# Performance work log

Measured on AMD Instinct MI355X. Metric: run time of the kernel, lower is better.

The kernel has to match this reference:

```python
import jax, jax.numpy as jnp
import numpy as np

B, S, D, NH, NKV, HD = 1, 2048, 4096, 32, 8, 128
SCALE = HD ** -0.5


def setup_inputs() -> dict:
    key = jax.random.key(0)
    ks = jax.random.split(key, 5)
    sd = D ** -0.5
    x = jax.random.normal(ks[0], (B, S, D), jnp.float32)
    Wq = jax.random.normal(ks[1], (D, NH * HD), jnp.float32) * sd
    Wk = jax.random.normal(ks[2], (D, NKV * HD), jnp.float32) * sd
    Wv = jax.random.normal(ks[3], (D, NKV * HD), jnp.float32) * sd
    Wo = jax.random.normal(ks[4], (NH * HD, D), jnp.float32) * sd
    # real rotary tables (rotate-half convention), shape [S, HD]
    inv_freq = 1.0 / (10000.0 ** (np.arange(0, HD, 2, dtype=np.float64) / HD))
    ang = np.outer(np.arange(S, dtype=np.float64), inv_freq)  # [S, HD//2]
    emb = np.concatenate([ang, ang], axis=-1)  # [S, HD]
    cos = jnp.asarray(np.cos(emb), jnp.float32)
    sin = jnp.asarray(np.sin(emb), jnp.float32)
    return dict(x=x, Wq=Wq, Wk=Wk, Wv=Wv, Wo=Wo, cos=cos, sin=sin)


def _rope(t, cos, sin):
    # t: [B,S,H,HD]; cos/sin: [S,HD]
    c = cos[None, :, None, :]
    s = sin[None, :, None, :]
    t1, t2 = jnp.split(t, 2, axis=-1)
    rot = jnp.concatenate([-t2, t1], axis=-1)
    return t * c + rot * s


def _to_i8(t):
    # per-vector absmax quantization over last dim
    scale = 127.0 / jnp.clip(jnp.max(jnp.abs(t), axis=-1, keepdims=True), 1e-5, None)
    q = jnp.clip(jnp.round(t * scale), -128.0, 127.0).astype(jnp.int8)
    return q, scale


def reference(x, Wq, Wk, Wv, Wo, cos, sin):
    q = (x @ Wq).reshape(B, S, NH, HD)
    k = (x @ Wk).reshape(B, S, NKV, HD)
    v = (x @ Wv).reshape(B, S, NKV, HD)
    q = _rope(q, cos, sin)
    k = _rope(k, cos, sin)
    q_i8, q_s = _to_i8(q)          # [B,S,NH,HD], [B,S,NH,1]
    k_i8, k_s = _to_i8(k)          # [B,S,NKV,HD], [B,S,NKV,1]
    rep = NH // NKV                # GQA expansion
    k_i8 = jnp.repeat(k_i8, rep, axis=2)
    k_s = jnp.repeat(k_s, rep, axis=2)
    v = jnp.repeat(v, rep, axis=2)
    # int8 QK^T accumulated in int32 (exact), then per-vector dequant
    scores = jnp.einsum('bshd,bthd->bhst', q_i8, k_i8,
                        preferred_element_type=jnp.int32).astype(jnp.float32)
    q_st = jnp.transpose(q_s, (0, 2, 1, 3))            # [B,NH,S,1]
    k_st = jnp.transpose(k_s, (0, 2, 3, 1))            # [B,NH,1,S]
    scores = scores * (SCALE / (q_st * k_st))
    # causal mask (seq > 1, no cache so total == S)
    mask = jnp.triu(jnp.full((S, S), -jnp.inf, jnp.float32), k=1)
    scores = scores + mask
    attn = jax.nn.softmax(scores, axis=-1)             # [B,NH,S,S]
    out = jnp.einsum('bhst,bthd->bshd', attn, v).reshape(B, S, NH * HD)
    return out @ Wo
```

## Files before the change

### kernel.cpp

```cpp
#include <hip/hip_runtime.h>
#include <hip/hip_bf16.h>

#define S_LEN 2048
#define DMODEL 4096
#define NH 32
#define NKV 8
#define HD 128
#define NQKV 6144
#define VOFF (DMODEL + NKV * HD)
#define ATT_SCALE_L2E 0.1275175213528852f

typedef __bf16 bf16x8 __attribute__((ext_vector_type(8)));
typedef __bf16 bf16x4 __attribute__((ext_vector_type(4)));
typedef float f32x4 __attribute__((ext_vector_type(4)));

template <bool B> struct BoolC { static constexpr bool value = B; };

__device__ __forceinline__ unsigned short f2b(float f) {
  union { float f; unsigned u; } a; a.f = f;
  unsigned u = a.u;
  return (unsigned short)((u + 0x7FFFu + ((u >> 16) & 1u)) >> 16);
}
__device__ __forceinline__ float b2f(unsigned short u) {
  union { unsigned u; float f; } a; a.u = (unsigned)u << 16; return a.f;
}

__device__ __forceinline__ void gl16(const unsigned short* g, unsigned short* l) {
  __builtin_amdgcn_global_load_lds(
      (const __attribute__((address_space(1))) unsigned int*)g,
      (__attribute__((address_space(3))) unsigned int*)l, 16, 0, 0);
}

__global__ __launch_bounds__(256) void k_prep(const float* __restrict__ x,
                                              const float* __restrict__ Wq,
                                              const float* __restrict__ Wk,
                                              const float* __restrict__ Wv,
                                              const float* __restrict__ Wo,
                                              unsigned short* __restrict__ xb,
                                              unsigned short* __restrict__ wqkv_t,
                                              unsigned short* __restrict__ wo_t) {
  __shared__ float tile[64][65];
  const int id = blockIdx.x;
  if (id >= 10240) {
    int i = (id - 10240) * 256 + threadIdx.x;
    float4 v = ((const float4*)x)[i];
    ushort4 o;
    o.x = f2b(v.x); o.y = f2b(v.y); o.z = f2b(v.z); o.w = f2b(v.w);
    ((ushort4*)xb)[i] = o;
    return;
  }
  const float* W;
  unsigned short* Wt;
  int N, bx, by;
  if (id < 4096)      { W = Wq; Wt = wqkv_t;                         N = 4096; bx = id & 63;          by = id >> 6; }
  else if (id < 5120) { W = Wk; Wt = wqkv_t + (size_t)4096 * 4096;   N = 1024; bx = (id - 4096) & 63; by = (id - 4096) >> 6; }
  else if (id < 6144) { W = Wv; Wt = wqkv_t + (size_t)5120 * 4096;   N = 1024; bx = (id - 5120) & 63; by = (id - 5120) >> 6; }
  else                { W = Wo; Wt = wo_t;                           N = 4096; bx = (id - 6144) & 63; by = (id - 6144) >> 6; }
  const int k0 = bx * 64, n0 = by * 64;
  const int tx = threadIdx.x & 31, ty = threadIdx.x >> 5;
#pragma unroll
  for (int i = 0; i < 8; ++i) {
    int k = ty + i * 8;
    const float* src = W + (size_t)(k0 + k) * N + n0;
    tile[k][tx] = src[tx];
    tile[k][tx + 32] = src[tx + 32];
  }
  __syncthreads();
  int kq = threadIdx.x & 15, nb = threadIdx.x >> 4;
#pragma unroll
  for (int i = 0; i < 4; ++i) {
    int n = nb + i * 16;
    ushort4 o;
    o.x = f2b(tile[kq * 4 + 0][n]);
    o.y = f2b(tile[kq * 4 + 1][n]);
    o.z = f2b(tile[kq * 4 + 2][n]);
    o.w = f2b(tile[kq * 4 + 3][n]);
    *(ushort4*)&Wt[(size_t)(n0 + n) * 4096 + k0 + kq * 4] = o;
  }
}

__global__ __launch_bounds__(256) void k_post(const unsigned short* __restrict__ qkv,
                                              const float* __restrict__ cost,
                                              const float* __restrict__ sint,
                                              unsigned short* __restrict__ q_int,
                                              float* __restrict__ q_ds_t,
                                              unsigned short* __restrict__ k_int,
                                              float* __restrict__ k_ds_t,
                                              unsigned short* __restrict__ v_t) {
  __shared__ unsigned short tile[64][65];
  const int id = blockIdx.x;
  if (id < 20480) {
    int y = id >> 11, s = id & 2047;
    int wv = threadIdx.x >> 6, l = threadIdx.x & 63;
    int hh = y * 4 + wv;
    const unsigned short* row = qkv + (size_t)s * NQKV;
    int off = (hh < NH) ? hh * HD : DMODEL + (hh - NH) * HD;
    float t1 = b2f(row[off + l]), t2 = b2f(row[off + 64 + l]);
    float c1 = cost[s * HD + l],      sn1 = sint[s * HD + l];
    float c2 = cost[s * HD + 64 + l], sn2 = sint[s * HD + 64 + l];
    float o1 = t1 * c1 - t2 * sn1;
    float o2 = t2 * c2 + t1 * sn2;
    float amax = fmaxf(fabsf(o1), fabsf(o2));
#pragma unroll
    for (int m = 1; m < 64; m <<= 1) amax = fmaxf(amax, __shfl_xor(amax, m));
    amax = fmaxf(amax, 1e-5f);
    float scale = 127.0f / amax;
    float dscale = amax * (1.0f / 127.0f);
    float v1 = fminf(fmaxf(rintf(o1 * scale), -128.f), 127.f);
    float v2 = fminf(fmaxf(rintf(o2 * scale), -128.f), 127.f);
    if (hh < NH) {
      unsigned short* dst = q_int + ((size_t)s * NH + hh) * HD;
      dst[l] = f2b(v1); dst[l + 64] = f2b(v2);
      if (l == 0) q_ds_t[(size_t)hh * S_LEN + s] = dscale;
    } else {
      int kh = hh - NH;
      unsigned short* dst = k_int + ((size_t)s * NKV + kh) * HD;
      dst[l] = f2b(v1); dst[l + 64] = f2b(v2);
      if (l == 0) k_ds_t[(size_t)kh * S_LEN + s] = dscale;
    }
    return;
  }
  int vid = id - 20480;
  int s0 = (vid & 31) * 64, d0 = ((vid >> 5) & 1) * 64, kvh = vid >> 6;
  int tx = threadIdx.x & 63, ty = threadIdx.x >> 6;
#pragma unroll
  for (int i = 0; i < 16; ++i) {
    int s = ty + i * 4;
    tile[s][tx] = qkv[(size_t)(s0 + s) * NQKV + VOFF + kvh * HD + d0 + tx];
  }
  __syncthreads();
#pragma unroll
  for (int i = 0; i < 16; ++i) {
    int d = ty + i * 4;
    v_t[((size_t)kvh * HD + d0 + d) * S_LEN + s0 + tx] = tile[tx][d];
  }
}

__global__ __launch_bounds__(512, 4) void k_g128x3(const unsigned short* __restrict__ A,
                                                   const unsigned short* __restrict__ B,
                                                   unsigned short* __restrict__ C,
                                                   int M, int N, int K) {
  constexpr int FN = 3;
  extern __shared__ __align__(16) unsigned short smem[];
  char* Sc = (char*)smem;
  const int tid = threadIdx.x;
  const int wvid = tid >> 6, l = tid & 63;
  const int wm = wvid >> 2, wn = wvid & 3;
  const int l15 = l & 15, l4 = l >> 4;

  const int cpx = gridDim.x >> 3;
  const int swz = (blockIdx.x & 7) * cpx + (blockIdx.x >> 3);
  const int mtiles = M >> 7;
  const int m0 = (swz % mtiles) * 128;
  const int n0 = (swz / mtiles) * (FN * 64);

  const int NT = K >> 6;

  const int rsw = (l15 & 7) << 4;
  const int a_base = (wm * 64 + l15) * 128;
  const int b_base = (wn * FN * 16 + l15) * 128;
  const int c0 = (l4 * 16) ^ rsw;
  const int c1 = (64 + l4 * 16) ^ rsw;

  const int srow = l >> 3;
  const int st_k8 = (l & 7) ^ (srow & 7);

  auto stA = [&](int tt) {
    if (tt >= NT) return;
    const unsigned short* g = A + (size_t)(m0 + wvid * 8 + srow) * K + tt * 64 + st_k8 * 8;
    char* lb = Sc + (tt & 1) * 16384 + wvid * 1024;
#pragma unroll
    for (int j = 0; j < 2; ++j)
      gl16(g + (size_t)(j * 64) * K, (unsigned short*)(lb + j * 8192));
  };
  auto stB = [&](int tt) {
    if (tt >= NT) return;
    const unsigned short* g = B + (size_t)(n0 + wvid * 8 + srow) * K + tt * 64 + st_k8 * 8;
    char* lb = Sc + 32768 + (tt & 1) * (FN * 8192) + wvid * 1024;
#pragma unroll
    for (int j = 0; j < FN; ++j)
      gl16(g + (size_t)(j * 64) * K, (unsigned short*)(lb + j * 8192));
  };

  f32x4 acc[4][FN] = {};

  stA(0); stB(0); stA(1);
  if (NT > 1) asm volatile("s_waitcnt vmcnt(2)" ::: "memory");
  else        asm volatile("s_waitcnt vmcnt(0)" ::: "memory");
  __builtin_amdgcn_s_barrier();

  for (int t = 0; t < NT; ++t) {
    const char* Ab = Sc + (t & 1) * 16384;
    const char* Bb = Sc + 32768 + (t & 1) * (FN * 8192);
    stB(t + 1);
    bf16x8 a[4], b[FN];
#pragma unroll
    for (int fm = 0; fm < 4; ++fm) a[fm] = *(const bf16x8*)(Ab + a_base + fm * 2048 + c0);
#pragma unroll
    for (int fn = 0; fn < FN; ++fn) b[fn] = *(const bf16x8*)(Bb + b_base + fn * 2048 + c0);
    __builtin_amdgcn_s_setprio(1);
#pragma unroll
    for (int fm = 0; fm < 4; ++fm)
#pragma unroll
      for (int fn = 0; fn < FN; ++fn)
        acc[fm][fn] = __builtin_amdgcn_mfma_f32_16x16x32_bf16(a[fm], b[fn], acc[fm][fn], 0, 0, 0);
    __builtin_amdgcn_s_setprio(0);
#pragma unroll
    for (int fm = 0; fm < 4; ++fm) a[fm] = *(const bf16x8*)(Ab + a_base + fm * 2048 + c1);
#pragma unroll
    for (int fn = 0; fn < FN; ++fn) b[fn] = *(const bf16x8*)(Bb + b_base + fn * 2048 + c1);
    __builtin_amdgcn_s_setprio(1);
#pragma unroll
    for (int fm = 0; fm < 4; ++fm)
#pragma unroll
      for (int fn = 0; fn < FN; ++fn)
        acc[fm][fn] = __builtin_amdgcn_mfma_f32_16x16x32_bf16(a[fm], b[fn], acc[fm][fn], 0, 0, 0);
    __builtin_amdgcn_s_setprio(0);
    __builtin_amdgcn_s_barrier();
    stA(t + 2);
    if (t + 1 < NT) {
      if (t + 1 == NT - 1) asm volatile("s_waitcnt vmcnt(0)" ::: "memory");
      else                 asm volatile("s_waitcnt vmcnt(2)" ::: "memory");
      __builtin_amdgcn_s_barrier();
    }
  }

#pragma unroll
  for (int fm = 0; fm < 4; ++fm) {
    int row0 = m0 + wm * 64 + fm * 16 + l4 * 4;
#pragma unroll
    for (int fn = 0; fn < FN; ++fn) {
      int col = n0 + wn * FN * 16 + fn * 16 + l15;
#pragma unroll
      for (int r = 0; r < 4; ++r)
        C[(size_t)(row0 + r) * N + col] = f2b(acc[fm][fn][r]);
    }
  }
}

__global__ __launch_bounds__(512, 4) void k_gksplit(const unsigned short* __restrict__ A,
                                                    const unsigned short* __restrict__ B,
                                                    float* __restrict__ C,
                                                    int M, int N, int K) {
  extern __shared__ __align__(16) unsigned short smem[];
  char* Sc = (char*)smem;
  const int tid = threadIdx.x;
  const int wvid = tid >> 6, l = tid & 63;
  const int wm = wvid & 1, wn = (wvid >> 1) & 1, wk = wvid >> 2;
  const int l15 = l & 15, l4 = l >> 4;

  const int cpx = gridDim.x >> 3;
  const int swz = (blockIdx.x & 7) * cpx + (blockIdx.x >> 3);
  const int mtiles = M >> 7;
  const int m0 = (swz % mtiles) * 128;
  const int n0 = (swz / mtiles) * 128;

  const int NT = K >> 6;

  const int rsw = (l15 & 7) << 4;
  const int a_base = (wm * 64 + l15) * 128;
  const int b_base = (wn * 64 + l15) * 128;
  const int ck = (wk * 64 + l4 * 16) ^ rsw;

  const int srow = l >> 3;
  const int st_k8 = (l & 7) ^ (srow & 7);

  auto stA = [&](int tt) {
    if (tt >= NT) return;
    const unsigned short* g = A + (size_t)(m0 + wvid * 8 + srow) * K + tt * 64 + st_k8 * 8;
    char* lb = Sc + (tt & 1) * 16384 + wvid * 1024;
#pragma unroll
    for (int j = 0; j < 2; ++j)
      gl16(g + (size_t)(j * 64) * K, (unsigned short*)(lb + j * 8192));
  };
  auto stB = [&](int tt) {
    if (tt >= NT) return;
    const unsigned short* g = B + (size_t)(n0 + wvid * 8 + srow) * K + tt * 64 + st_k8 * 8;
    char* lb = Sc + 32768 + (tt & 1) * 16384 + wvid * 1024;
#pragma unroll
    for (int j = 0; j < 2; ++j)
      gl16(g + (size_t)(j * 64) * K, (unsigned short*)(lb + j * 8192));
  };

  f32x4 acc[4][4] = {};

  stA(0); stB(0); stA(1);
  if (NT > 1) asm volatile("s_waitcnt vmcnt(2)" ::: "memory");
  else        asm volatile("s_waitcnt vmcnt(0)" ::: "memory");
  __builtin_amdgcn_s_barrier();

  for (int t = 0; t < NT; ++t) {
    const char* Ab = Sc + (t & 1) * 16384;
    const char* Bb = Sc + 32768 + (t & 1) * 16384;
    stB(t + 1);
    bf16x8 a[4], b[4];
#pragma unroll
    for (int fm = 0; fm < 4; ++fm) a[fm] = *(const bf16x8*)(Ab + a_base + fm * 2048 + ck);
#pragma unroll
    for (int fn = 0; fn < 4; ++fn) b[fn] = *(const bf16x8*)(Bb + b_base + fn * 2048 + ck);
    __builtin_amdgcn_s_setprio(1);
#pragma unroll
    for (int fm = 0; fm < 4; ++fm)
#pragma unroll
      for (int fn = 0; fn < 4; ++fn)
        acc[fm][fn] = __builtin_amdgcn_mfma_f32_16x16x32_bf16(a[fm], b[fn], acc[fm][fn], 0, 0, 0);
    __builtin_amdgcn_s_setprio(0);
    __builtin_amdgcn_s_barrier();
    stA(t + 2);
    if (t + 1 < NT) {
      if (t + 1 == NT - 1) asm volatile("s_waitcnt vmcnt(0)" ::: "memory");
      else                 asm volatile("s_waitcnt vmcnt(2)" ::: "memory");
      __builtin_amdgcn_s_barrier();
    }
  }

  char* xch = Sc + (wm * 2 + wn) * 16384;
  if (wk == 1) {
#pragma unroll
    for (int fm = 0; fm < 4; ++fm)
#pragma unroll
      for (int fn = 0; fn < 4; ++fn)
        *(f32x4*)(xch + (fm * 4 + fn) * 1024 + l * 16) = acc[fm][fn];
  }
  __syncthreads();
  if (wk == 0) {
#pragma unroll
    for (int fm = 0; fm < 4; ++fm) {
      int row0 = m0 + wm * 64 + fm * 16 + l4 * 4;
#pragma unroll
      for (int fn = 0; fn < 4; ++fn) {
        f32x4 o = *(const f32x4*)(xch + (fm * 4 + fn) * 1024 + l * 16);
        int col = n0 + wn * 64 + fn * 16 + l15;
#pragma unroll
        for (int r = 0; r < 4; ++r)
          C[(size_t)(row0 + r) * N + col] = acc[fm][fn][r] + o[r];
      }
    }
  }
}

__global__ __launch_bounds__(512, 4) void k_attn(const unsigned short* __restrict__ q_int,
                                                 const float* __restrict__ q_ds_t,
                                                 const unsigned short* __restrict__ k_int,
                                                 const float* __restrict__ k_ds_t,
                                                 const unsigned short* __restrict__ v_t,
                                                 unsigned short* __restrict__ o_bf) {
  __shared__ __align__(16) unsigned short K_lds[2][8192];
  __shared__ __align__(16) unsigned short V_lds[2][8192];
  __shared__ __align__(16) unsigned short P_lds[8][1024];

  const int bid = blockIdx.x;
  const int kvh = bid & 7;
  const int qt = 63 - (bid >> 3);
  const int tid = threadIdx.x, wv = tid >> 6, l = tid & 63;
  const int l15 = l & 15, l4 = l >> 4;
  const int h = kvh * 4 + (wv & 3);
  const int rh = wv >> 2;

  auto stage = [&](int b, int kt) {
    const unsigned short* kB = k_int + (size_t)kt * 64 * (NKV * HD) + kvh * HD;
    const unsigned short* vB = v_t + (size_t)kvh * HD * S_LEN + (size_t)kt * 64;
#pragma unroll
    for (int j = 0; j < 2; ++j) {
      int wi = j * 8 + wv;
      int slot = wi * 64 + l;
      int key = slot >> 4;
      int colb = ((slot & 15) * 16) ^ ((key & 7) << 4);
      gl16(kB + key * (NKV * HD) + (colb >> 1), &K_lds[b][wi * 512]);
      int d = slot >> 3;
      int ckb = ((slot & 7) * 16) ^ ((d & 7) << 4);
      gl16(vB + (size_t)d * S_LEN + (ckb >> 1), &V_lds[b][wi * 512]);
    }
  };

  const int qrow_lo = qt * 32 + rh * 16;
  const int qg = qrow_lo + l15;
  const int crow = qrow_lo + l4 * 4;

  bf16x8 qf[4];
  {
    const unsigned short* qp = q_int + ((size_t)qg * NH + h) * HD + l4 * 8;
#pragma unroll
    for (int kd = 0; kd < 4; ++kd) qf[kd] = *(const bf16x8*)(qp + kd * 32);
  }
  const float qsS = ATT_SCALE_L2E * q_ds_t[(size_t)h * S_LEN + qg];

  float m_run = -3.0e38f, l_run = 0.f;
  f32x4 o_acc[8] = {};

  const int nkt = (qt >> 1) + 1;
  stage(0, 0);
  __syncthreads();

  const int psw = (l15 & 7) << 4;

  auto tileBody = [&](auto mc, int kt) {
    constexpr bool MASKED = decltype(mc)::value;
    const int cur = kt & 1;
    f32x4 ksd[4];
    {
      const f32x4* kdp = (const f32x4*)(k_ds_t + (size_t)kvh * S_LEN + kt * 64 + l4 * 4);
#pragma unroll
      for (int nt = 0; nt < 4; ++nt) ksd[nt] = kdp[nt * 4];
    }
    if (kt + 1 < nkt) stage(cur ^ 1, kt + 1);

    f32x4 sacc[4] = {};
#pragma unroll
    for (int nt = 0; nt < 4; ++nt) {
      int key = nt * 16 + l15;
#pragma unroll
      for (int kd = 0; kd < 4; ++kd) {
        int byte = key * 256 + kd * 64 + l4 * 16;
        byte ^= (key & 7) << 4;
        bf16x8 kf = *(const bf16x8*)((const char*)&K_lds[cur][0] + byte);
        sacc[nt] = __builtin_amdgcn_mfma_f32_16x16x32_bf16(kf, qf[kd], sacc[nt], 0, 0, 0);
      }
    }

    float p[4][4];
    float tmax = -3.0e38f;
#pragma unroll
    for (int nt = 0; nt < 4; ++nt) {
#pragma unroll
      for (int r = 0; r < 4; ++r) {
        float sc = sacc[nt][r] * (qsS * ksd[nt][r]);
        if constexpr (MASKED) {
          int keyg = kt * 64 + nt * 16 + l4 * 4 + r;
          sc = (keyg <= qg) ? sc : -3.0e38f;
        }
        p[nt][r] = sc;
        tmax = fmaxf(tmax, sc);
      }
    }
    tmax = fmaxf(tmax, __shfl_xor(tmax, 16));
    tmax = fmaxf(tmax, __shfl_xor(tmax, 32));

    float nm = fmaxf(m_run, tmax);
    bool need = tmax > m_run + 11.0f;
    if (__ballot(need)) {
      float corr = __builtin_amdgcn_exp2f(m_run - nm);
      m_run = nm;
      l_run *= corr;
      float cq[4];
#pragma unroll
      for (int r = 0; r < 4; ++r) cq[r] = __shfl(corr, (l & 48) | (l4 * 4 + r));
#pragma unroll
      for (int dt = 0; dt < 8; ++dt)
#pragma unroll
        for (int r = 0; r < 4; ++r) o_acc[dt][r] *= cq[r];
    }

    float psum = 0.f;
#pragma unroll
    for (int nt = 0; nt < 4; ++nt)
#pragma unroll
      for (int r = 0; r < 4; ++r) {
        float e = __builtin_amdgcn_exp2f(p[nt][r] - m_run);
        p[nt][r] = e;
        psum += e;
      }
    psum += __shfl_xor(psum, 16);
    psum += __shfl_xor(psum, 32);
    l_run += psum;

#pragma unroll
    for (int nt = 0; nt < 4; ++nt) {
      bf16x4 pk;
      pk[0] = (__bf16)p[nt][0]; pk[1] = (__bf16)p[nt][1];
      pk[2] = (__bf16)p[nt][2]; pk[3] = (__bf16)p[nt][3];
      int bw = l15 * 128 + ((nt * 32 + l4 * 8) ^ psw);
      *(bf16x4*)((char*)&P_lds[wv][0] + bw) = pk;
    }
    bf16x8 pa[2];
#pragma unroll
    for (int kc = 0; kc < 2; ++kc) {
      int br = l15 * 128 + ((kc * 64 + l4 * 16) ^ psw);
      pa[kc] = *(const bf16x8*)((const char*)&P_lds[wv][0] + br);
    }

#pragma unroll
    for (int dt = 0; dt < 8; ++dt) {
      int d = dt * 16 + l15;
      int swzv = (d & 7) << 4;
#pragma unroll
      for (int kc = 0; kc < 2; ++kc) {
        int byte = d * 128 + ((kc * 64 + l4 * 16) ^ swzv);
        bf16x8 vb = *(const bf16x8*)((const char*)&V_lds[cur][0] + byte);
        o_acc[dt] = __builtin_amdgcn_mfma_f32_16x16x32_bf16(pa[kc], vb, o_acc[dt], 0, 0, 0);
      }
    }
    __syncthreads();
  };

  for (int kt = 0; kt + 1 < nkt; ++kt) tileBody(BoolC<false>{}, kt);
  tileBody(BoolC<true>{}, nkt - 1);

  float inv = 1.0f / l_run;
  float invq[4];
#pragma unroll
  for (int r = 0; r < 4; ++r) invq[r] = __shfl(inv, (l & 48) | (l4 * 4 + r));
#pragma unroll
  for (int dt = 0; dt < 8; ++dt)
#pragma unroll
    for (int r = 0; r < 4; ++r)
      o_bf[(size_t)(crow + r) * (NH * HD) + h * HD + dt * 16 + l15] =
          f2b(o_acc[dt][r] * invq[r]);
}

extern "C" void kernel_launch(void* const* d_in, const int* in_sizes, int n_in,
                              void* d_out, int out_size, void* d_ws, size_t ws_size,
                              hipStream_t stream) {
  const float* x    = (const float*)d_in[0];
  const float* Wq   = (const float*)d_in[1];
  const float* Wk   = (const float*)d_in[2];
  const float* Wv   = (const float*)d_in[3];
  const float* Wo   = (const float*)d_in[4];
  const float* cost = (const float*)d_in[5];
  const float* sint = (const float*)d_in[6];
  float* out = (float*)d_out;
  char* ws = (char*)d_ws;

  unsigned short* xb     = (unsigned short*)(ws);
  unsigned short* wqkv_t = (unsigned short*)(ws + 16777216);
  unsigned short* wo_t   = (unsigned short*)(ws + 67108864);
  unsigned short* qkv    = (unsigned short*)(ws + 100663296);
  unsigned short* q_int  = (unsigned short*)(ws + 150994944);
  unsigned short* k_int  = (unsigned short*)(ws + 167772160);
  float*          q_ds_t = (float*)(ws + 176160768);
  float*          k_ds_t = (float*)(ws + 176422912);
  unsigned short* o_bf   = (unsigned short*)(ws + 176488448);
  unsigned short* v_t    = (unsigned short*)(ws);

  hipFuncSetAttribute((const void*)k_g128x3,
                      hipFuncAttributeMaxDynamicSharedMemorySize, 81920);
  hipFuncSetAttribute((const void*)k_gksplit,
                      hipFuncAttributeMaxDynamicSharedMemorySize, 65536);

  k_prep<<<dim3(18432), 256, 0, stream>>>(x, Wq, Wk, Wv, Wo, xb, wqkv_t, wo_t);
  k_g128x3<<<dim3(512), 512, 81920, stream>>>(xb, wqkv_t, qkv, 2048, 6144, 4096);
  k_post<<<dim3(20992), 256, 0, stream>>>(qkv, cost, sint, q_int, q_ds_t, k_int, k_ds_t, v_t);
  k_attn<<<dim3(512), 512, 0, stream>>>(q_int, q_ds_t, k_int, k_ds_t, v_t, o_bf);
  k_gksplit<<<dim3(512), 512, 65536, stream>>>(o_bf, wo_t, out, 2048, 4096, 4096);
}
```

Before: 306.6 us.

## Split K across wave groups in QKV GEMM with LDS reduction

The QKV projection GEMM now splits each 64-wide K step between two groups of four waves instead of tiling waves 2x4 over M/N. Each wave holds a 64x96 accumulator tile, and the two K-halves are summed through LDS in the epilogue before the bf16 store. The goal is to cut LDS fragment reads per MFMA, since larger per-wave tiles mean more operand reuse, and to halve the read/compute phases per iteration. The cost is double the accumulator registers, which may strain occupancy at 4 blocks per CU, plus an extra LDS exchange with barriers in the epilogue.

```diff
diff --git a/kernel.cpp b/kernel.cpp
--- a/kernel.cpp
+++ b/kernel.cpp
@@ -136,31 +136,29 @@
   }
 }
 
-__global__ __launch_bounds__(512, 4) void k_g128x3(const unsigned short* __restrict__ A,
+__global__ __launch_bounds__(512, 4) void k_g192ks(const unsigned short* __restrict__ A,
                                                    const unsigned short* __restrict__ B,
                                                    unsigned short* __restrict__ C,
                                                    int M, int N, int K) {
-  constexpr int FN = 3;
   extern __shared__ __align__(16) unsigned short smem[];
   char* Sc = (char*)smem;
   const int tid = threadIdx.x;
   const int wvid = tid >> 6, l = tid & 63;
-  const int wm = wvid >> 2, wn = wvid & 3;
+  const int wm = wvid & 1, wn = (wvid >> 1) & 1, wk = wvid >> 2;
   const int l15 = l & 15, l4 = l >> 4;
 
   const int cpx = gridDim.x >> 3;
   const int swz = (blockIdx.x & 7) * cpx + (blockIdx.x >> 3);
   const int mtiles = M >> 7;
   const int m0 = (swz % mtiles) * 128;
-  const int n0 = (swz / mtiles) * (FN * 64);
+  const int n0 = (swz / mtiles) * 192;
 
   const int NT = K >> 6;
 
   const int rsw = (l15 & 7) << 4;
   const int a_base = (wm * 64 + l15) * 128;
-  const int b_base = (wn * FN * 16 + l15) * 128;
-  const int c0 = (l4 * 16) ^ rsw;
-  const int c1 = (64 + l4 * 16) ^ rsw;
+  const int b_base = (wn * 96 + l15) * 128;
+  const int ck = (wk * 64 + l4 * 16) ^ rsw;
 
   const int srow = l >> 3;
   const int st_k8 = (l & 7) ^ (srow & 7);
@@ -176,13 +174,13 @@
   auto stB = [&](int tt) {
     if (tt >= NT) return;
     const unsigned short* g = B + (size_t)(n0 + wvid * 8 + srow) * K + tt * 64 + st_k8 * 8;
-    char* lb = Sc + 32768 + (tt & 1) * (FN * 8192) + wvid * 1024;
-#pragma unroll
-    for (int j = 0; j < FN; ++j)
+    char* lb = Sc + 32768 + (tt & 1) * 24576 + wvid * 1024;
+#pragma unroll
+    for (int j = 0; j < 3; ++j)
       gl16(g + (size_t)(j * 64) * K, (unsigned short*)(lb + j * 8192));
   };
 
-  f32x4 acc[4][FN] = {};
+  f32x4 acc[4][6] = {};
 
   stA(0); stB(0); stA(1);
   if (NT > 1) asm volatile("s_waitcnt vmcnt(2)" ::: "memory");
@@ -191,29 +189,18 @@
 
   for (int t = 0; t < NT; ++t) {
     const char* Ab = Sc + (t & 1) * 16384;
-    const char* Bb = Sc + 32768 + (t & 1) * (FN * 8192);
+    const char* Bb = Sc + 32768 + (t & 1) * 24576;
     stB(t + 1);
-    bf16x8 a[4], b[FN];
-#pragma unroll
-    for (int fm = 0; fm < 4; ++fm) a[fm] = *(const bf16x8*)(Ab + a_base + fm * 2048 + c0);
-#pragma unroll
-    for (int fn = 0; fn < FN; ++fn) b[fn] = *(const bf16x8*)(Bb + b_base + fn * 2048 + c0);
+    bf16x8 a[4], b[6];
+#pragma unroll
+    for (int fm = 0; fm < 4; ++fm) a[fm] = *(const bf16x8*)(Ab + a_base + fm * 2048 + ck);
+#pragma unroll
+    for (int fn = 0; fn < 6; ++fn) b[fn] = *(const bf16x8*)(Bb + b_base + fn * 2048 + ck);
     __builtin_amdgcn_s_setprio(1);
 #pragma unroll
     for (int fm = 0; fm < 4; ++fm)
 #pragma unroll
-      for (int fn = 0; fn < FN; ++fn)
-        acc[fm][fn] = __builtin_amdgcn_mfma_f32_16x16x32_bf16(a[fm], b[fn], acc[fm][fn], 0, 0, 0);
-    __builtin_amdgcn_s_setprio(0);
-#pragma unroll
-    for (int fm = 0; fm < 4; ++fm) a[fm] = *(const bf16x8*)(Ab + a_base + fm * 2048 + c1);
-#pragma unroll
-    for (int fn = 0; fn < FN; ++fn) b[fn] = *(const bf16x8*)(Bb + b_base + fn * 2048 + c1);
-    __builtin_amdgcn_s_setprio(1);
-#pragma unroll
-    for (int fm = 0; fm < 4; ++fm)
-#pragma unroll
-      for (int fn = 0; fn < FN; ++fn)
+      for (int fn = 0; fn < 6; ++fn)
         acc[fm][fn] = __builtin_amdgcn_mfma_f32_16x16x32_bf16(a[fm], b[fn], acc[fm][fn], 0, 0, 0);
     __builtin_amdgcn_s_setprio(0);
     __builtin_amdgcn_s_barrier();
@@ -225,16 +212,34 @@
     }
   }
 
-#pragma unroll
-  for (int fm = 0; fm < 4; ++fm) {
-    int row0 = m0 + wm * 64 + fm * 16 + l4 * 4;
-#pragma unroll
-    for (int fn = 0; fn < FN; ++fn) {
-      int col = n0 + wn * FN * 16 + fn * 16 + l15;
-#pragma unroll
-      for (int r = 0; r < 4; ++r)
-        C[(size_t)(row0 + r) * N + col] = f2b(acc[fm][fn][r]);
-    }
+  const int pairid = wm * 2 + wn;
+  char* xch = Sc + pairid * 12288;
+#pragma unroll
+  for (int h = 0; h < 2; ++h) {
+    if (wk == 1) {
+#pragma unroll
+      for (int fm2 = 0; fm2 < 2; ++fm2)
+#pragma unroll
+        for (int fn = 0; fn < 6; ++fn)
+          *(f32x4*)(xch + (fm2 * 6 + fn) * 1024 + l * 16) = acc[h * 2 + fm2][fn];
+    }
+    __syncthreads();
+    if (wk == 0) {
+#pragma unroll
+      for (int fm2 = 0; fm2 < 2; ++fm2) {
+        int fm = h * 2 + fm2;
+        int row0 = m0 + wm * 64 + fm * 16 + l4 * 4;
+#pragma unroll
+        for (int fn = 0; fn < 6; ++fn) {
+          f32x4 o = *(const f32x4*)(xch + (fm2 * 6 + fn) * 1024 + l * 16);
+          int col = n0 + wn * 96 + fn * 16 + l15;
+#pragma unroll
+          for (int r = 0; r < 4; ++r)
+            C[(size_t)(row0 + r) * N + col] = f2b(acc[fm][fn][r] + o[r]);
+        }
+      }
+    }
+    __syncthreads();
   }
 }
 
@@ -532,13 +537,13 @@
   unsigned short* o_bf   = (unsigned short*)(ws + 176488448);
   unsigned short* v_t    = (unsigned short*)(ws);
 
-  hipFuncSetAttribute((const void*)k_g128x3,
+  hipFuncSetAttribute((const void*)k_g192ks,
                       hipFuncAttributeMaxDynamicSharedMemorySize, 81920);
   hipFuncSetAttribute((const void*)k_gksplit,
                       hipFuncAttributeMaxDynamicSharedMemorySize, 65536);
 
   k_prep<<<dim3(18432), 256, 0, stream>>>(x, Wq, Wk, Wv, Wo, xb, wqkv_t, wo_t);
-  k_g128x3<<<dim3(512), 512, 81920, stream>>>(xb, wqkv_t, qkv, 2048, 6144, 4096);
+  k_g192ks<<<dim3(512), 512, 81920, stream>>>(xb, wqkv_t, qkv, 2048, 6144, 4096);
   k_post<<<dim3(20992), 256, 0, stream>>>(qkv, cost, sint, q_int, q_ds_t, k_int, k_ds_t, v_t);
   k_attn<<<dim3(512), 512, 0, stream>>>(q_int, q_ds_t, k_int, k_ds_t, v_t, o_bf);
   k_gksplit<<<dim3(512), 512, 65536, stream>>>(o_bf, wo_t, out, 2048, 4096, 4096);
```

After: 724.9 us. 136% more time.

## Use int8 MFMA for QK^T with int8 Q/K storage

Applied to the files above, without the earlier changes.

Stores quantized Q and K as int8 instead of bf16-encoded integers and computes attention scores with the i32 16x16x64 int8 MFMA. This halves K tile staging traffic and LDS footprint, halves the QK MFMA count, and makes the int32 accumulation exact as in the reference. The K staging layout and swizzle are reworked to fit 128-byte rows, loaded with one 16-byte global-to-LDS transfer per thread.

```diff
diff --git a/kernel.cpp b/kernel.cpp
--- a/kernel.cpp
+++ b/kernel.cpp
@@ -13,6 +13,7 @@
 typedef __bf16 bf16x8 __attribute__((ext_vector_type(8)));
 typedef __bf16 bf16x4 __attribute__((ext_vector_type(4)));
 typedef float f32x4 __attribute__((ext_vector_type(4)));
+typedef int i32x4 __attribute__((ext_vector_type(4)));
 
 template <bool B> struct BoolC { static constexpr bool value = B; };
 
@@ -25,7 +26,7 @@
   union { unsigned u; float f; } a; a.u = (unsigned)u << 16; return a.f;
 }
 
-__device__ __forceinline__ void gl16(const unsigned short* g, unsigned short* l) {
+__device__ __forceinline__ void gl16(const void* g, void* l) {
   __builtin_amdgcn_global_load_lds(
       (const __attribute__((address_space(1))) unsigned int*)g,
       (__attribute__((address_space(3))) unsigned int*)l, 16, 0, 0);
@@ -82,9 +83,9 @@
 __global__ __launch_bounds__(256) void k_post(const unsigned short* __restrict__ qkv,
                                               const float* __restrict__ cost,
                                               const float* __restrict__ sint,
-                                              unsigned short* __restrict__ q_int,
+                                              signed char* __restrict__ q_i8,
                                               float* __restrict__ q_ds_t,
-                                              unsigned short* __restrict__ k_int,
+                                              signed char* __restrict__ k_i8,
                                               float* __restrict__ k_ds_t,
                                               unsigned short* __restrict__ v_t) {
   __shared__ unsigned short tile[64][65];
@@ -109,13 +110,13 @@
     float v1 = fminf(fmaxf(rintf(o1 * scale), -128.f), 127.f);
     float v2 = fminf(fmaxf(rintf(o2 * scale), -128.f), 127.f);
     if (hh < NH) {
-      unsigned short* dst = q_int + ((size_t)s * NH + hh) * HD;
-      dst[l] = f2b(v1); dst[l + 64] = f2b(v2);
+      signed char* dst = q_i8 + ((size_t)s * NH + hh) * HD;
+      dst[l] = (signed char)v1; dst[l + 64] = (signed char)v2;
       if (l == 0) q_ds_t[(size_t)hh * S_LEN + s] = dscale;
     } else {
       int kh = hh - NH;
-      unsigned short* dst = k_int + ((size_t)s * NKV + kh) * HD;
-      dst[l] = f2b(v1); dst[l + 64] = f2b(v2);
+      signed char* dst = k_i8 + ((size_t)s * NKV + kh) * HD;
+      dst[l] = (signed char)v1; dst[l + 64] = (signed char)v2;
       if (l == 0) k_ds_t[(size_t)kh * S_LEN + s] = dscale;
     }
     return;
@@ -339,13 +340,13 @@
   }
 }
 
-__global__ __launch_bounds__(512, 4) void k_attn(const unsigned short* __restrict__ q_int,
+__global__ __launch_bounds__(512, 4) void k_attn(const signed char* __restrict__ q_i8,
                                                  const float* __restrict__ q_ds_t,
-                                                 const unsigned short* __restrict__ k_int,
+                                                 const signed char* __restrict__ k_i8,
                                                  const float* __restrict__ k_ds_t,
                                                  const unsigned short* __restrict__ v_t,
                                                  unsigned short* __restrict__ o_bf) {
-  __shared__ __align__(16) unsigned short K_lds[2][8192];
+  __shared__ __align__(16) signed char K_lds[2][8192];
   __shared__ __align__(16) unsigned short V_lds[2][8192];
   __shared__ __align__(16) unsigned short P_lds[8][1024];
 
@@ -358,15 +359,17 @@
   const int rh = wv >> 2;
 
   auto stage = [&](int b, int kt) {
-    const unsigned short* kB = k_int + (size_t)kt * 64 * (NKV * HD) + kvh * HD;
+    {
+      int key = tid >> 3, g = tid & 7;
+      int colb = (g * 16) ^ ((key & 7) << 4);
+      const signed char* src = k_i8 + ((size_t)(kt * 64 + key) * NKV + kvh) * HD + colb;
+      gl16(src, &K_lds[b][tid * 16]);
+    }
     const unsigned short* vB = v_t + (size_t)kvh * HD * S_LEN + (size_t)kt * 64;
 #pragma unroll
     for (int j = 0; j < 2; ++j) {
       int wi = j * 8 + wv;
       int slot = wi * 64 + l;
-      int key = slot >> 4;
-      int colb = ((slot & 15) * 16) ^ ((key & 7) << 4);
-      gl16(kB + key * (NKV * HD) + (colb >> 1), &K_lds[b][wi * 512]);
       int d = slot >> 3;
       int ckb = ((slot & 7) * 16) ^ ((d & 7) << 4);
       gl16(vB + (size_t)d * S_LEN + (ckb >> 1), &V_lds[b][wi * 512]);
@@ -377,11 +380,11 @@
   const int qg = qrow_lo + l15;
   const int crow = qrow_lo + l4 * 4;
 
-  bf16x8 qf[4];
+  i32x4 qf[2];
   {
-    const unsigned short* qp = q_int + ((size_t)qg * NH + h) * HD + l4 * 8;
-#pragma unroll
-    for (int kd = 0; kd < 4; ++kd) qf[kd] = *(const bf16x8*)(qp + kd * 32);
+    const signed char* qp = q_i8 + ((size_t)qg * NH + h) * HD + l4 * 16;
+    qf[0] = *(const i32x4*)(qp);
+    qf[1] = *(const i32x4*)(qp + 64);
   }
   const float qsS = ATT_SCALE_L2E * q_ds_t[(size_t)h * S_LEN + qg];
 
@@ -405,16 +408,16 @@
     }
     if (kt + 1 < nkt) stage(cur ^ 1, kt + 1);
 
-    f32x4 sacc[4] = {};
+    i32x4 sacc[4] = {};
 #pragma unroll
     for (int nt = 0; nt < 4; ++nt) {
       int key = nt * 16 + l15;
 #pragma unroll
-      for (int kd = 0; kd < 4; ++kd) {
-        int byte = key * 256 + kd * 64 + l4 * 16;
+      for (int kd = 0; kd < 2; ++kd) {
+        int byte = key * 128 + kd * 64 + l4 * 16;
         byte ^= (key & 7) << 4;
-        bf16x8 kf = *(const bf16x8*)((const char*)&K_lds[cur][0] + byte);
-        sacc[nt] = __builtin_amdgcn_mfma_f32_16x16x32_bf16(kf, qf[kd], sacc[nt], 0, 0, 0);
+        i32x4 kf = *(const i32x4*)(&K_lds[cur][0] + byte);
+        sacc[nt] = __builtin_amdgcn_mfma_i32_16x16x64_i8(kf, qf[kd], sacc[nt], 0, 0, 0);
       }
     }
 
@@ -424,7 +427,7 @@
     for (int nt = 0; nt < 4; ++nt) {
 #pragma unroll
       for (int r = 0; r < 4; ++r) {
-        float sc = sacc[nt][r] * (qsS * ksd[nt][r]);
+        float sc = (float)sacc[nt][r] * (qsS * ksd[nt][r]);
         if constexpr (MASKED) {
           int keyg = kt * 64 + nt * 16 + l4 * 4 + r;
           sc = (keyg <= qg) ? sc : -3.0e38f;
@@ -525,8 +528,8 @@
   unsigned short* wqkv_t = (unsigned short*)(ws + 16777216);
   unsigned short* wo_t   = (unsigned short*)(ws + 67108864);
   unsigned short* qkv    = (unsigned short*)(ws + 100663296);
-  unsigned short* q_int  = (unsigned short*)(ws + 150994944);
-  unsigned short* k_int  = (unsigned short*)(ws + 167772160);
+  signed char*    q_i8   = (signed char*)(ws + 150994944);
+  signed char*    k_i8   = (signed char*)(ws + 167772160);
   float*          q_ds_t = (float*)(ws + 176160768);
   float*          k_ds_t = (float*)(ws + 176422912);
   unsigned short* o_bf   = (unsigned short*)(ws + 176488448);
@@ -539,7 +542,7 @@
 
   k_prep<<<dim3(18432), 256, 0, stream>>>(x, Wq, Wk, Wv, Wo, xb, wqkv_t, wo_t);
   k_g128x3<<<dim3(512), 512, 81920, stream>>>(xb, wqkv_t, qkv, 2048, 6144, 4096);
-  k_post<<<dim3(20992), 256, 0, stream>>>(qkv, cost, sint, q_int, q_ds_t, k_int, k_ds_t, v_t);
-  k_attn<<<dim3(512), 512, 0, stream>>>(q_int, q_ds_t, k_int, k_ds_t, v_t, o_bf);
+  k_post<<<dim3(20992), 256, 0, stream>>>(qkv, cost, sint, q_i8, q_ds_t, k_i8, k_ds_t, v_t);
+  k_attn<<<dim3(512), 512, 0, stream>>>(q_i8, q_ds_t, k_i8, k_ds_t, v_t, o_bf);
   k_gksplit<<<dim3(512), 512, 65536, stream>>>(o_bf, wo_t, out, 2048, 4096, 4096);
 }
```

After: 288.5 us. 5.9% less time.
